# Kernel optimization log

Hardware: AMD Instinct MI355X
Metric: run time of the kernel (lower is better)

## Reference

```python
import jax, jax.numpy as jnp
import numpy as np

N = 20000      # nodes
L = 64         # seq_length
E = 64         # emb_size
V = 30000      # vocab_size
HG = 128       # gnn_hidden_size
HT = 128       # text_hidden_size
NE = 640000    # edges
EPS = 1e-12


def _normalize(x):
    # F.normalize(x, p=2, dim=1) on [N, E, L]
    n = jnp.sqrt(jnp.sum(x * x, axis=1, keepdims=True))
    return x / jnp.maximum(n, EPS)


def gcn_conv(x, W, b, src_idx, dst_idx, n_nodes):
    # PyG GCNConv: add self-loops, symmetric normalization D^-1/2 (A+I) D^-1/2 (X W) + b
    h = x @ W                                            # [N, out]
    deg = jnp.zeros((n_nodes,), h.dtype).at[dst_idx].add(1.0) + 1.0  # incl. self-loop
    dinv = jax.lax.rsqrt(deg)
    norm = dinv[src_idx] * dinv[dst_idx]                 # [NE]
    msg = h[src_idx] * norm[:, None]                     # gather + scale
    out = jnp.zeros_like(h).at[dst_idx].add(msg)         # scatter-add to targets
    out = out + h * (dinv * dinv)[:, None]               # self-loop term
    return out + b


def setup_inputs() -> dict:
    key = jax.random.key(0)
    ks = jax.random.split(key, 12)
    rn = lambda k, shape: jax.random.normal(k, shape, jnp.float32) * 0.02
    return {
        "src": jax.random.randint(ks[0], (N, L), 0, V),
        "seg": jax.random.randint(ks[1], (N, L), 0, 3),
        "edge_index": jax.random.randint(ks[2], (2, NE), 0, N),
        "src_emb": rn(ks[3], (V, E)),
        "seg_emb": rn(ks[4], (3, E)),
        "w": jnp.ones((L,), jnp.float32),
        "Wq1": rn(ks[5], (E, HT)), "bq1": jnp.zeros((HT,), jnp.float32),
        "Wq2": rn(ks[6], (HT, E)), "bq2": jnp.zeros((E,), jnp.float32),
        "Wg1": rn(ks[7], (E, HG)), "bg1": jnp.zeros((HG,), jnp.float32),
        "Wg2": rn(ks[8], (HG, E)), "bg2": jnp.zeros((E,), jnp.float32),
        "Wl": rn(ks[9], (E, E)),   "bl": jnp.zeros((E,), jnp.float32),
    }


def reference(src, seg, edge_index, src_emb, seg_emb, w, Wq1, bq1, Wq2, bq2,
              Wg1, bg1, Wg2, bg2, Wl, bl):
    # --- LiteratureEmbedding ---
    se = src_emb[src]                 # [N, L, E]
    ge = seg_emb[seg]                 # [N, L, E]
    sv = se.reshape(-1, E, L)         # raw view (matches torch .view, not transpose)
    gv = ge.reshape(-1, E, L)
    f = (_normalize(w * sv) + _normalize(gv)).sum(-1)   # [N, E]
    # --- query MLP ---
    x = jax.nn.relu(f @ Wq1 + bq1) @ Wq2 + bq2
    # --- two GCN layers ---
    si, di = edge_index[0], edge_index[1]
    x = jax.nn.relu(gcn_conv(x, Wg1, bg1, si, di, N))
    x = jax.nn.relu(gcn_conv(x, Wg2, bg2, si, di, N))
    # --- output linear (dropout is identity in eval) ---
    return x @ Wl + bl
```

## Files before the change

kernel.cpp:

```cpp
#include <hip/hip_runtime.h>

#if defined(__has_builtin)
#if __has_builtin(__builtin_amdgcn_readlane)
#define READLANE(v, l) __builtin_amdgcn_readlane((v), (l))
#else
#define READLANE(v, l) __shfl((v), (l))
#endif
#else
#define READLANE(v, l) __shfl((v), (l))
#endif
__device__ __forceinline__ float readlane_f(float v, int l) {
    return __uint_as_float(READLANE(__float_as_uint(v), l));
}

__device__ __forceinline__ unsigned short f2bf(float x) {
    unsigned u = __float_as_uint(x);
    u += 0x7FFFu + ((u >> 16) & 1u);
    return (unsigned short)(u >> 16);
}
__device__ __forceinline__ float bfl(unsigned u) { return __uint_as_float(u << 16); }
__device__ __forceinline__ float bfh(unsigned u) { return __uint_as_float(u & 0xFFFF0000u); }

#define CAPLOG 8

__global__ __launch_bounds__(256) void prep0_k(
    const float* __restrict__ src_emb, unsigned short* __restrict__ sbf, int ve,
    const int* __restrict__ si, const int* __restrict__ di,
    int* __restrict__ cursor, int* __restrict__ edge_off, int ne, int eB)
{
    const int b = blockIdx.x, t = threadIdx.x;
    if (b < eB) {
        int i = b * 256 + t;
        if (i < ne) {
            int d = di[i];
            int pos = atomicAdd(cursor + d, 1);
            edge_off[((long)d << CAPLOG) + pos] = si[i] << 7;
        }
        return;
    }
    int i = ((b - eB) * 256 + t) * 4;
    if (i + 3 < ve) {
        float4 v = *(const float4*)&src_emb[i];
        ushort4 u;
        u.x = f2bf(v.x); u.y = f2bf(v.y); u.z = f2bf(v.z); u.w = f2bf(v.w);
        *(ushort4*)&sbf[i] = u;
    } else {
        for (; i < ve; ++i) sbf[i] = f2bf(src_emb[i]);
    }
}

__global__ __launch_bounds__(256) void prep1_k(
    const int* __restrict__ src, const int* __restrict__ seg,
    const unsigned short* __restrict__ sbf, const float* __restrict__ seg_emb,
    const float* __restrict__ wvec, float* __restrict__ f, int nN)
{
    __shared__ float scr[4][16 * 66];
    const int t = threadIdx.x;
    const int wid = t >> 6, q = t & 63;
    const long n = (long)blockIdx.x * 4 + wid;
    if (n >= nN) return;
    const int grp = q >> 4, c = q & 15;

    const int off = src[n * 64 + q] << 7;
    const int sg  = seg[n * 64 + q];
    const float e0 = seg_emb[q], e1 = seg_emb[64 + q], e2 = seg_emb[128 + q];
    const char* base = (const char*)sbf;

    uint2 dreg[16];
    #pragma unroll
    for (int i = 0; i < 16; ++i) {
        int ro = __shfl(off, i * 4 + grp);
        dreg[i] = *(const uint2*)(base + (ro + c * 8));
    }

    float t0 = 0.f, t1 = 0.f, t2 = 0.f, t3 = 0.f;
    #pragma unroll
    for (int i = 0; i < 16; ++i) {
        float v0 = bfl(dreg[i].x);
        float v1 = bfh(dreg[i].x);
        float v2 = bfl(dreg[i].y);
        float v3 = bfh(dreg[i].y);
        t0 += v0 * v0; t1 += v1 * v1; t2 += v2 * v2; t3 += v3 * v3;
    }
    t0 += __shfl_xor(t0, 16); t0 += __shfl_xor(t0, 32);
    t1 += __shfl_xor(t1, 16); t1 += __shfl_xor(t1, 32);
    t2 += __shfl_xor(t2, 16); t2 += __shfl_xor(t2, 32);
    t3 += __shfl_xor(t3, 16); t3 += __shfl_xor(t3, 32);

    const float4 wv = *(const float4*)&wvec[c * 4];
    float4 cf;
    cf.x = wv.x / fmaxf(fabsf(wv.x) * sqrtf(t0), 1e-12f);
    cf.y = wv.y / fmaxf(fabsf(wv.y) * sqrtf(t1), 1e-12f);
    cf.z = wv.z / fmaxf(fabsf(wv.z) * sqrtf(t2), 1e-12f);
    cf.w = wv.w / fmaxf(fabsf(wv.w) * sqrtf(t3), 1e-12f);

    unsigned long long b0 = __ballot(sg == 0);
    unsigned long long b1 = __ballot(sg == 1);
    float n0 = (float)__popcll(b0), n1 = (float)__popcll(b1);
    float n2 = 64.f - n0 - n1;
    float g2 = n0 * e0 * e0 + n1 * e1 * e1 + n2 * e2 * e2;
    float rg = 1.f / fmaxf(sqrtf(g2), 1e-12f);
    float p0 = e0 * rg, p1 = e1 * rg, p2 = e2 * rg;
    #pragma unroll
    for (int m = 1; m < 64; m <<= 1) {
        p0 += __shfl_xor(p0, m);
        p1 += __shfl_xor(p1, m);
        p2 += __shfl_xor(p2, m);
    }

    float* sw = scr[wid];
    #pragma unroll
    for (int i = 0; i < 16; ++i) {
        float po = bfl(dreg[i].x) * cf.x + bfh(dreg[i].x) * cf.y
                 + bfl(dreg[i].y) * cf.z + bfh(dreg[i].y) * cf.w;
        sw[c * 66 + i * 4 + grp] = po;
    }
    float out = 0.f;
    #pragma unroll
    for (int c2 = 0; c2 < 16; ++c2)
        out += sw[c2 * 66 + q];

    const float dg = (sg == 0) ? p0 : ((sg == 1) ? p1 : p2);
    f[n * 64 + q] = out + dg;
}

#define ACC8(d, a, b)                                                    \
    { (a).x += bfl((d).x); (a).y += bfh((d).x);                          \
      (a).z += bfl((d).y); (a).w += bfh((d).y);                          \
      (b).x += bfl((d).z); (b).y += bfh((d).z);                          \
      (b).z += bfl((d).w); (b).w += bfh((d).w); }

__device__ __forceinline__ void csr_gather16(const char* __restrict__ hb,
                                             const int* __restrict__ eo,
                                             int dn, int j, int zoff,
                                             float4& s0, float4& s1)
{
    const int grp = j >> 3;
    const int col = (j & 7) << 4;
    float4 a0 = make_float4(0.f, 0.f, 0.f, 0.f), a1 = a0;
    float4 b0 = a0, b1 = a0;
    for (int e = 0; e < dn; e += 64) {
        const int cnt = min(dn - e, 64);
        const int eoff = (e + j < dn) ? eo[e + j] : zoff;
        int m = 0;
        for (; m + 16 <= cnt; m += 16) {
            int o0 = __shfl(eoff, m + grp);
            int o1 = __shfl(eoff, m + 8 + grp);
            uint4 d0 = *(const uint4*)(hb + (o0 + col));
            uint4 d1 = *(const uint4*)(hb + (o1 + col));
            ACC8(d0, a0, a1); ACC8(d1, b0, b1);
        }
        for (; m < cnt; m += 8) {
            int o = __shfl(eoff, m + grp);
            uint4 d = *(const uint4*)(hb + (o + col));
            ACC8(d, a0, a1);
        }
    }
    a0.x += b0.x; a0.y += b0.y; a0.z += b0.z; a0.w += b0.w;
    a1.x += b1.x; a1.y += b1.y; a1.z += b1.z; a1.w += b1.w;
    #pragma unroll
    for (int m = 8; m < 64; m <<= 1) {
        a0.x += __shfl_xor(a0.x, m); a0.y += __shfl_xor(a0.y, m);
        a0.z += __shfl_xor(a0.z, m); a0.w += __shfl_xor(a0.w, m);
        a1.x += __shfl_xor(a1.x, m); a1.y += __shfl_xor(a1.y, m);
        a1.z += __shfl_xor(a1.z, m); a1.w += __shfl_xor(a1.w, m);
    }
    s0 = a0; s1 = a1;
}

__device__ __forceinline__ void bf_row16(const char* hb, long rowoff, int col,
                                         float4& v0, float4& v1) {
    uint4 d = *(const uint4*)(hb + rowoff + col);
    v0.x = bfl(d.x); v0.y = bfh(d.x); v0.z = bfl(d.y); v0.w = bfh(d.y);
    v1.x = bfl(d.z); v1.y = bfh(d.z); v1.z = bfl(d.w); v1.w = bfh(d.w);
}

template <bool S2_BIAS>
__device__ __forceinline__ void dense_pair_body(
    float* Wh, float* F, float* H,
    const float* __restrict__ W1, const float* __restrict__ b1,
    const float* __restrict__ W2, const float* __restrict__ b2,
    const int* __restrict__ deg, unsigned short* __restrict__ out,
    int row0, int nrows, int t)
{
    for (int i = t * 4; i < 32 * 128; i += 1024)
        *(float4*)&Wh[i] = *(const float4*)&W1[i];
    __syncthreads();

    const int jg = t & 31, rslot = t >> 5;
    const int j0 = jg * 4;
    float4 acc0, acc1;
    {
        float4 b4 = *(const float4*)&b1[j0];
        acc0 = b4; acc1 = b4;
    }
    #pragma unroll 2
    for (int k = 0; k < 32; k += 4) {
        float4 w0 = *(float4*)&Wh[(k + 0) * 128 + j0];
        float4 w1 = *(float4*)&Wh[(k + 1) * 128 + j0];
        float4 w2 = *(float4*)&Wh[(k + 2) * 128 + j0];
        float4 w3 = *(float4*)&Wh[(k + 3) * 128 + j0];
        float4 fa = *(float4*)&F[rslot * 64 + k];
        float4 fb = *(float4*)&F[(rslot + 8) * 64 + k];
        acc0.x += fa.x * w0.x + fa.y * w1.x + fa.z * w2.x + fa.w * w3.x;
        acc0.y += fa.x * w0.y + fa.y * w1.y + fa.z * w2.y + fa.w * w3.y;
        acc0.z += fa.x * w0.z + fa.y * w1.z + fa.z * w2.z + fa.w * w3.z;
        acc0.w += fa.x * w0.w + fa.y * w1.w + fa.z * w2.w + fa.w * w3.w;
        acc1.x += fb.x * w0.x + fb.y * w1.x + fb.z * w2.x + fb.w * w3.x;
        acc1.y += fb.x * w0.y + fb.y * w1.y + fb.z * w2.y + fb.w * w3.y;
        acc1.z += fb.x * w0.z + fb.y * w1.z + fb.z * w2.z + fb.w * w3.z;
        acc1.w += fb.x * w0.w + fb.y * w1.w + fb.z * w2.w + fb.w * w3.w;
    }
    __syncthreads();
    for (int i = t * 4; i < 32 * 128; i += 1024)
        *(float4*)&Wh[i] = *(const float4*)&W1[32 * 128 + i];
    __syncthreads();
    #pragma unroll 2
    for (int k = 0; k < 32; k += 4) {
        float4 w0 = *(float4*)&Wh[(k + 0) * 128 + j0];
        float4 w1 = *(float4*)&Wh[(k + 1) * 128 + j0];
        float4 w2 = *(float4*)&Wh[(k + 2) * 128 + j0];
        float4 w3 = *(float4*)&Wh[(k + 3) * 128 + j0];
        float4 fa = *(float4*)&F[rslot * 64 + 32 + k];
        float4 fb = *(float4*)&F[(rslot + 8) * 64 + 32 + k];
        acc0.x += fa.x * w0.x + fa.y * w1.x + fa.z * w2.x + fa.w * w3.x;
        acc0.y += fa.x * w0.y + fa.y * w1.y + fa.z * w2.y + fa.w * w3.y;
        acc0.z += fa.x * w0.z + fa.y * w1.z + fa.z * w2.z + fa.w * w3.z;
        acc0.w += fa.x * w0.w + fa.y * w1.w + fa.z * w2.w + fa.w * w3.w;
        acc1.x += fb.x * w0.x + fb.y * w1.x + fb.z * w2.x + fb.w * w3.x;
        acc1.y += fb.x * w0.y + fb.y * w1.y + fb.z * w2.y + fb.w * w3.y;
        acc1.z += fb.x * w0.z + fb.y * w1.z + fb.z * w2.z + fb.w * w3.z;
        acc1.w += fb.x * w0.w + fb.y * w1.w + fb.z * w2.w + fb.w * w3.w;
    }
    {
        float4 v;
        v.x = fmaxf(acc0.x, 0.f); v.y = fmaxf(acc0.y, 0.f);
        v.z = fmaxf(acc0.z, 0.f); v.w = fmaxf(acc0.w, 0.f);
        *(float4*)&H[rslot * 128 + j0] = v;
        v.x = fmaxf(acc1.x, 0.f); v.y = fmaxf(acc1.y, 0.f);
        v.z = fmaxf(acc1.z, 0.f); v.w = fmaxf(acc1.w, 0.f);
        *(float4*)&H[(rslot + 8) * 128 + j0] = v;
    }
    __syncthreads();

    for (int i = t * 4; i < 64 * 64; i += 1024)
        *(float4*)&Wh[i] = *(const float4*)&W2[i];
    __syncthreads();
    const int jg2 = t & 15, r2 = t >> 4;
    const int j02 = jg2 * 4;
    float4 acc = S2_BIAS ? *(const float4*)&b2[j02]
                         : make_float4(0.f, 0.f, 0.f, 0.f);
    #pragma unroll 2
    for (int k = 0; k < 64; k += 4) {
        float4 w0 = *(float4*)&Wh[(k + 0) * 64 + j02];
        float4 w1 = *(float4*)&Wh[(k + 1) * 64 + j02];
        float4 w2 = *(float4*)&Wh[(k + 2) * 64 + j02];
        float4 w3 = *(float4*)&Wh[(k + 3) * 64 + j02];
        float4 fq = *(float4*)&H[r2 * 128 + k];
        acc.x += fq.x * w0.x + fq.y * w1.x + fq.z * w2.x + fq.w * w3.x;
        acc.y += fq.x * w0.y + fq.y * w1.y + fq.z * w2.y + fq.w * w3.y;
        acc.z += fq.x * w0.z + fq.y * w1.z + fq.z * w2.z + fq.w * w3.z;
        acc.w += fq.x * w0.w + fq.y * w1.w + fq.z * w2.w + fq.w * w3.w;
    }
    __syncthreads();
    for (int i = t * 4; i < 64 * 64; i += 1024)
        *(float4*)&Wh[i] = *(const float4*)&W2[64 * 64 + i];
    __syncthreads();
    #pragma unroll 2
    for (int k = 0; k < 64; k += 4) {
        float4 w0 = *(float4*)&Wh[(k + 0) * 64 + j02];
        float4 w1 = *(float4*)&Wh[(k + 1) * 64 + j02];
        float4 w2 = *(float4*)&Wh[(k + 2) * 64 + j02];
        float4 w3 = *(float4*)&Wh[(k + 3) * 64 + j02];
        float4 fq = *(float4*)&H[r2 * 128 + 64 + k];
        acc.x += fq.x * w0.x + fq.y * w1.x + fq.z * w2.x + fq.w * w3.x;
        acc.y += fq.x * w0.y + fq.y * w1.y + fq.z * w2.y + fq.w * w3.y;
        acc.z += fq.x * w0.z + fq.y * w1.z + fq.z * w2.z + fq.w * w3.z;
        acc.w += fq.x * w0.w + fq.y * w1.w + fq.z * w2.w + fq.w * w3.w;
    }
    const int r = row0 + r2;
    if (r < nrows) {
        float sc = rsqrtf((float)deg[r] + 1.0f);
        ushort4 v;
        v.x = f2bf(acc.x * sc); v.y = f2bf(acc.y * sc);
        v.z = f2bf(acc.z * sc); v.w = f2bf(acc.w * sc);
        *(ushort4*)&out[(long)r * 64 + j02] = v;
    }
}

template <bool S2_BIAS>
__global__ __launch_bounds__(256, 5) void fused2_k(
    const float* __restrict__ in, const float* __restrict__ W1,
    const float* __restrict__ b1, const float* __restrict__ W2,
    const float* __restrict__ b2, const int* __restrict__ deg,
    unsigned short* __restrict__ out, int nrows)
{
    __shared__ __align__(16) float Wh[32 * 128];
    __shared__ __align__(16) float F[16 * 64];
    __shared__ __align__(16) float H[16 * 128];
    const int t = threadIdx.x;
    const int row0 = blockIdx.x * 16;

    for (int i = t * 4; i < 16 * 64; i += 1024) {
        int r = i >> 6;
        float4 v = make_float4(0.f, 0.f, 0.f, 0.f);
        if (row0 + r < nrows) v = *(const float4*)&in[(long)row0 * 64 + i];
        *(float4*)&F[i] = v;
    }
    dense_pair_body<S2_BIAS>(Wh, F, H, W1, b1, W2, b2, deg, out, row0, nrows, t);
}

__global__ __launch_bounds__(256, 5) void gcnfused_k(
    const unsigned short* __restrict__ C, const int* __restrict__ deg,
    const int* __restrict__ edge_off,
    const float* __restrict__ W1, const float* __restrict__ b1,
    const float* __restrict__ W2, unsigned short* __restrict__ out,
    int nrows, int zoff)
{
    __shared__ __align__(16) float Wh[32 * 128];
    __shared__ __align__(16) float F[16 * 64];
    __shared__ __align__(16) float H[16 * 128];
    const int t = threadIdx.x;
    const int row0 = blockIdx.x * 16;
    const int wv = t >> 6, j = t & 63;
    const int col = (j & 7) << 4;

    const char* hb = (const char*)C;
    #pragma unroll
    for (int i = 0; i < 4; ++i) {
        const int r = wv * 4 + i;
        const int node = row0 + r;
        if (node < nrows) {
            float4 s0, s1, v0, v1;
            csr_gather16(hb, edge_off + ((long)node << CAPLOG),
                         deg[node], j, zoff, s0, s1);
            bf_row16(hb, (long)node << 7, col, v0, v1);
            float dv = rsqrtf((float)deg[node] + 1.0f);
            if ((j >> 3) == 0) {
                float4 ra, rb;
                ra.x = dv * (v0.x + s0.x); ra.y = dv * (v0.y + s0.y);
                ra.z = dv * (v0.z + s0.z); ra.w = dv * (v0.w + s0.w);
                rb.x = dv * (v1.x + s1.x); rb.y = dv * (v1.y + s1.y);
                rb.z = dv * (v1.z + s1.z); rb.w = dv * (v1.w + s1.w);
                *(float4*)&F[r * 64 + j * 8]     = ra;
                *(float4*)&F[r * 64 + j * 8 + 4] = rb;
            }
        } else if ((j >> 3) == 0) {
            *(float4*)&F[r * 64 + j * 8]     = make_float4(0.f, 0.f, 0.f, 0.f);
            *(float4*)&F[r * 64 + j * 8 + 4] = make_float4(0.f, 0.f, 0.f, 0.f);
        }
    }
    dense_pair_body<false>(Wh, F, H, W1, b1, W2, nullptr, deg, out, row0, nrows, t);
}

__global__ __launch_bounds__(256) void gatherout_k(
    const unsigned short* __restrict__ hp, const int* __restrict__ deg,
    const int* __restrict__ edge_off,
    const float* __restrict__ bg2, const float* __restrict__ Wl,
    const float* __restrict__ bl, float* __restrict__ out, int n, int zoff)
{
    __shared__ __align__(16) float WlL[64 * 64];
    __shared__ __align__(16) float vS[4][64];
    const int t = threadIdx.x;
    for (int i = t * 4; i < 64 * 64; i += 1024)
        *(float4*)&WlL[i] = *(const float4*)&Wl[i];
    __syncthreads();

    const int row0 = blockIdx.x * 16;
    const int wv = t >> 6, j = t & 63;
    const int col = (j & 7) << 4;
    const char* hb = (const char*)hp;
    const float blj = bl[j];
    const float4 bgA = *(const float4*)&bg2[(j & 7) * 8];
    const float4 bgB = *(const float4*)&bg2[(j & 7) * 8 + 4];

    #pragma unroll
    for (int i = 0; i < 4; ++i) {
        const int node = row0 + wv * 4 + i;
        if (node >= n) continue;
        float4 s0, s1, v0, v1;
        csr_gather16(hb, edge_off + ((long)node << CAPLOG),
                     deg[node], j, zoff, s0, s1);
        bf_row16(hb, (long)node << 7, col, v0, v1);
        const float dv = rsqrtf((float)deg[node] + 1.0f);
        float4 fa, fb;
        fa.x = fmaxf(dv * (v0.x + s0.x) + bgA.x, 0.f);
        fa.y = fmaxf(dv * (v0.y + s0.y) + bgA.y, 0.f);
        fa.z = fmaxf(dv * (v0.z + s0.z) + bgA.z, 0.f);
        fa.w = fmaxf(dv * (v0.w + s0.w) + bgA.w, 0.f);
        fb.x = fmaxf(dv * (v1.x + s1.x) + bgB.x, 0.f);
        fb.y = fmaxf(dv * (v1.y + s1.y) + bgB.y, 0.f);
        fb.z = fmaxf(dv * (v1.z + s1.z) + bgB.z, 0.f);
        fb.w = fmaxf(dv * (v1.w + s1.w) + bgB.w, 0.f);
        if ((j >> 3) == 0) {
            *(float4*)&vS[wv][j * 8]     = fa;
            *(float4*)&vS[wv][j * 8 + 4] = fb;
        }
        const float v = vS[wv][j];

        float o = blj;
        #pragma unroll 4
        for (int k = 0; k < 64; k += 4) {
            float vk0 = readlane_f(v, k + 0);
            float vk1 = readlane_f(v, k + 1);
            float vk2 = readlane_f(v, k + 2);
            float vk3 = readlane_f(v, k + 3);
            o += vk0 * WlL[(k + 0) * 64 + j] + vk1 * WlL[(k + 1) * 64 + j]
               + vk2 * WlL[(k + 2) * 64 + j] + vk3 * WlL[(k + 3) * 64 + j];
        }
        out[(long)node * 64 + j] = o;
    }
}

extern "C" void kernel_launch(void* const* d_in, const int* in_sizes, int n_in,
                              void* d_out, int out_size, void* d_ws, size_t ws_size,
                              hipStream_t stream) {
    const int*   src     = (const int*)  d_in[0];
    const int*   seg     = (const int*)  d_in[1];
    const int*   ei      = (const int*)  d_in[2];
    const float* src_emb = (const float*)d_in[3];
    const float* seg_emb = (const float*)d_in[4];
    const float* w       = (const float*)d_in[5];
    const float* Wq1     = (const float*)d_in[6];
    const float* bq1     = (const float*)d_in[7];
    const float* Wq2     = (const float*)d_in[8];
    const float* bq2     = (const float*)d_in[9];
    const float* Wg1     = (const float*)d_in[10];
    const float* bg1     = (const float*)d_in[11];
    const float* Wg2     = (const float*)d_in[12];
    const float* bg2     = (const float*)d_in[13];
    const float* Wl      = (const float*)d_in[14];
    const float* bl      = (const float*)d_in[15];
    float* out = (float*)d_out;

    const int N  = in_sizes[0] / 64;
    const int NE = in_sizes[2] / 2;
    const int VE = in_sizes[3];
    const int* si = ei;
    const int* di = ei + NE;

    const size_t Npad  = ((size_t)N + 3) & ~(size_t)3;
    const size_t VEpad = ((size_t)VE + 7) & ~(size_t)7;
    int* cursor   = (int*)d_ws;
    int* edge_off = cursor + Npad;
    unsigned short* sbf = (unsigned short*)(edge_off + ((size_t)N << CAPLOG));
    float* A32 = (float*)(sbf + VEpad);
    unsigned short* Cbf = (unsigned short*)(A32 + (size_t)N * 64);
    unsigned short* Abf = Cbf + (size_t)N * 64 + 64;
    const int zoff = N << 7;

    dim3 b256(256);
    const int convB = (VE + 1023) / 1024;
    const int eB    = (NE + 255) / 256;
    const int nB    = (N + 3) / 4;
    const int fB    = (N + 15) / 16;

    hipMemsetAsync(cursor, 0, Npad * sizeof(int), stream);
    hipMemsetAsync(Cbf + (size_t)N * 64, 0, 128, stream);
    hipMemsetAsync(Abf + (size_t)N * 64, 0, 128, stream);

    prep0_k<<<eB + convB, b256, 0, stream>>>(src_emb, sbf, VE,
                                             si, di, cursor, edge_off, NE, eB);

    prep1_k<<<nB, b256, 0, stream>>>(src, seg, sbf, seg_emb, w, A32, N);

    fused2_k<true><<<fB, b256, 0, stream>>>(A32, Wq1, bq1, Wq2, bq2,
                                            cursor, Cbf, N);

    gcnfused_k<<<fB, b256, 0, stream>>>(Cbf, cursor, edge_off,
                                        Wg1, bg1, Wg2, Abf, N, zoff);

    gatherout_k<<<fB, b256, 0, stream>>>(Abf, cursor, edge_off, bg2,
                                         Wl, bl, out, N, zoff);
}
```

Measured before the change: 225.0 us.

## Build per-node edge lists via two-level bucket sort instead of global atomics

Replaces the per-edge global atomicAdd on a per-node cursor with a bucketed counting sort. Edges are histogrammed into 64-node buckets, scanned, scattered as packed (local dst, src) pairs, and then each bucket is expanded in shared memory into the padded per-node edge list plus a degree array. The aim is to cut global atomic contention and the scattered writes to edge_off. The cost is three extra kernel launches and an extra pass over the edge pairs through global memory. Edges beyond 256 per node are dropped, and the packing assumes source indices fit in 20 bits.

After: 215.5 us (median of 2 runs). 4.2% less time.

```diff
diff --git a/kernel.cpp b/kernel.cpp
--- a/kernel.cpp
+++ b/kernel.cpp
@@ -22,23 +22,80 @@
 __device__ __forceinline__ float bfh(unsigned u) { return __uint_as_float(u & 0xFFFF0000u); }
 
 #define CAPLOG 8
-
-__global__ __launch_bounds__(256) void prep0_k(
-    const float* __restrict__ src_emb, unsigned short* __restrict__ sbf, int ve,
-    const int* __restrict__ si, const int* __restrict__ di,
-    int* __restrict__ cursor, int* __restrict__ edge_off, int ne, int eB)
-{
-    const int b = blockIdx.x, t = threadIdx.x;
-    if (b < eB) {
-        int i = b * 256 + t;
-        if (i < ne) {
-            int d = di[i];
-            int pos = atomicAdd(cursor + d, 1);
-            edge_off[((long)d << CAPLOG) + pos] = si[i] << 7;
+#define EPB 10
+
+__global__ __launch_bounds__(256) void hist_k(
+    const int* __restrict__ di, int ne, int* __restrict__ bhist)
+{
+    __shared__ int lh[512];
+    const int t = threadIdx.x;
+    for (int i = t; i < 512; i += 256) lh[i] = 0;
+    __syncthreads();
+    const int base = blockIdx.x * (256 * EPB);
+    #pragma unroll
+    for (int r = 0; r < EPB; ++r) {
+        int i = base + r * 256 + t;
+        if (i < ne) atomicAdd(&lh[di[i] >> 6], 1);
+    }
+    __syncthreads();
+    for (int i = t; i < 512; i += 256)
+        if (lh[i]) atomicAdd(&bhist[i], lh[i]);
+}
+
+__global__ __launch_bounds__(256) void scan_k(
+    const int* __restrict__ bhist, int* __restrict__ boff,
+    int* __restrict__ bcur, int nb,
+    unsigned* __restrict__ Cz, unsigned* __restrict__ Az)
+{
+    __shared__ int sh[512];
+    const int t = threadIdx.x;
+    for (int i = t; i < 512; i += 256) sh[i] = (i < nb) ? bhist[i] : 0;
+    __syncthreads();
+    if (t == 0) {
+        int run = 0;
+        for (int i = 0; i < nb; ++i) { int v = sh[i]; sh[i] = run; run += v; }
+    }
+    __syncthreads();
+    for (int i = t; i < 512; i += 256)
+        if (i < nb) { boff[i] = sh[i]; bcur[i] = sh[i]; }
+    if (t < 32) { Cz[t] = 0u; Az[t] = 0u; }
+}
+
+__global__ __launch_bounds__(256) void prep0b_k(
+    const int* __restrict__ si, const int* __restrict__ di, int ne,
+    int* __restrict__ bcur, unsigned* __restrict__ pairs, int pB,
+    const float* __restrict__ src_emb, unsigned short* __restrict__ sbf, int ve)
+{
+    const int t = threadIdx.x;
+    if ((int)blockIdx.x < pB) {
+        __shared__ int lh[512];
+        __shared__ int lbase[512];
+        for (int i = t; i < 512; i += 256) lh[i] = 0;
+        __syncthreads();
+        int bb[EPB], rk[EPB];
+        unsigned pk[EPB];
+        const int base = blockIdx.x * (256 * EPB);
+        #pragma unroll
+        for (int r = 0; r < EPB; ++r) {
+            int i = base + r * 256 + t;
+            if (i < ne) {
+                int d = di[i], s = si[i];
+                int b = d >> 6;
+                bb[r] = b;
+                rk[r] = atomicAdd(&lh[b], 1);
+                pk[r] = ((unsigned)(d & 63) << 20) | (unsigned)s;
+            } else bb[r] = -1;
         }
+        __syncthreads();
+        for (int i = t; i < 512; i += 256)
+            if (lh[i]) lbase[i] = atomicAdd(&bcur[i], lh[i]);
+        __syncthreads();
+        #pragma unroll
+        for (int r = 0; r < EPB; ++r)
+            if (bb[r] >= 0) pairs[lbase[bb[r]] + rk[r]] = pk[r];
         return;
     }
-    int i = ((b - eB) * 256 + t) * 4;
+    int i = (((int)blockIdx.x - pB) * 256 + t) * 4;
     if (i + 3 < ve) {
         float4 v = *(const float4*)&src_emb[i];
         ushort4 u;
@@ -46,6 +103,42 @@
         *(ushort4*)&sbf[i] = u;
     } else {
         for (; i < ve; ++i) sbf[i] = f2bf(src_emb[i]);
+    }
+}
+
+__global__ __launch_bounds__(256) void binfill_k(
+    const unsigned* __restrict__ pairs, const int* __restrict__ bhist,
+    const int* __restrict__ boff, int* __restrict__ edge_off,
+    int* __restrict__ deg, int nN)
+{
+    __shared__ int cntL[64];
+    __shared__ int slotsL[64 * 256];
+    const int t = threadIdx.x;
+    const int b = blockIdx.x;
+    if (t < 64) cntL[t] = 0;
+    __syncthreads();
+    const int ne_b = bhist[b];
+    const int st   = boff[b];
+    for (int k = t; k < ne_b; k += 256) {
+        unsigned pk = pairs[st + k];
+        int dl = (int)(pk >> 20);
+        int s  = (int)(pk & 0xFFFFFu);
+        int p  = atomicAdd(&cntL[dl], 1);
+        if (p < 256) slotsL[dl * 256 + p] = s << 7;
+    }
+    __syncthreads();
+    if (t < 64) {
+        int node = (b << 6) + t;
+        if (node < nN) deg[node] = cntL[t];
+    }
+    const int wv = t >> 6, j = t & 63;
+    const int dl = wv * 16 + (j >> 2);
+    const int k0 = j & 3;
+    const int node = (b << 6) + dl;
+    if (node < nN) {
+        const int c = min(cntL[dl], 256);
+        for (int k = k0; k < c; k += 4)
+            edge_off[((long)node << CAPLOG) + k] = slotsL[dl * 256 + k];
     }
 }
 
@@ -438,12 +531,17 @@
     const int VE = in_sizes[3];
     const int* si = ei;
     const int* di = ei + NE;
-
-    const size_t Npad  = ((size_t)N + 3) & ~(size_t)3;
+    const int NB = (N + 63) >> 6;
+
+    const size_t NEpad = ((size_t)NE + 3) & ~(size_t)3;
     const size_t VEpad = ((size_t)VE + 7) & ~(size_t)7;
-    int* cursor   = (int*)d_ws;
-    int* edge_off = cursor + Npad;
-    unsigned short* sbf = (unsigned short*)(edge_off + ((size_t)N << CAPLOG));
+    int* bhist = (int*)d_ws;
+    int* boff  = bhist + 512;
+    int* bcur  = boff + 512;
+    int* deg   = bcur + 512;
+    int* edge_off = deg + (((size_t)N + 3) & ~(size_t)3);
+    unsigned* pairs = (unsigned*)(edge_off + ((size_t)N << CAPLOG));
+    unsigned short* sbf = (unsigned short*)(pairs + NEpad);
     float* A32 = (float*)(sbf + VEpad);
     unsigned short* Cbf = (unsigned short*)(A32 + (size_t)N * 64);
     unsigned short* Abf = Cbf + (size_t)N * 64 + 64;
@@ -451,25 +549,28 @@
 
     dim3 b256(256);
     const int convB = (VE + 1023) / 1024;
-    const int eB    = (NE + 255) / 256;
+    const int eBig  = (NE + 256 * EPB - 1) / (256 * EPB);
     const int nB    = (N + 3) / 4;
     const int fB    = (N + 15) / 16;
 
-    hipMemsetAsync(cursor, 0, Npad * sizeof(int), stream);
-    hipMemsetAsync(Cbf + (size_t)N * 64, 0, 128, stream);
-    hipMemsetAsync(Abf + (size_t)N * 64, 0, 128, stream);
-
-    prep0_k<<<eB + convB, b256, 0, stream>>>(src_emb, sbf, VE,
-                                             si, di, cursor, edge_off, NE, eB);
+    hipMemsetAsync(bhist, 0, 512 * sizeof(int), stream);
+
+    hist_k<<<eBig, b256, 0, stream>>>(di, NE, bhist);
+    scan_k<<<1, b256, 0, stream>>>(bhist, boff, bcur, NB,
+                                   (unsigned*)(Cbf + (size_t)N * 64),
+                                   (unsigned*)(Abf + (size_t)N * 64));
+    prep0b_k<<<eBig + convB, b256, 0, stream>>>(si, di, NE, bcur, pairs, eBig,
+                                                src_emb, sbf, VE);
+    binfill_k<<<NB, b256, 0, stream>>>(pairs, bhist, boff, edge_off, deg, N);
 
     prep1_k<<<nB, b256, 0, stream>>>(src, seg, sbf, seg_emb, w, A32, N);
 
     fused2_k<true><<<fB, b256, 0, stream>>>(A32, Wq1, bq1, Wq2, bq2,
-                                            cursor, Cbf, N);
-
-    gcnfused_k<<<fB, b256, 0, stream>>>(Cbf, cursor, edge_off,
+                                            deg, Cbf, N);
+
+    gcnfused_k<<<fB, b256, 0, stream>>>(Cbf, deg, edge_off,
                                         Wg1, bg1, Wg2, Abf, N, zoff);
 
-    gatherout_k<<<fB, b256, 0, stream>>>(Abf, cursor, edge_off, bg2,
+    gatherout_k<<<fB, b256, 0, stream>>>(Abf, deg, edge_off, bg2,
                                          Wl, bl, out, N, zoff);
 }
```
